# Kernel optimization log

Measured on AMD Instinct MI355X. Metric: run time of the kernel, lower is better.

## Reference

```python
import jax, jax.numpy as jnp
import numpy as np

SEQ_DIM = 256
PAIR_DIM = 128
N_HEADS = 8
HIDDEN = 32
B, L = 4, 512


def layer_norm(x, gamma, beta, eps=1e-5):
    mu = jnp.mean(x, axis=-1, keepdims=True)
    var = jnp.var(x, axis=-1, keepdims=True)
    return (x - mu) * jax.lax.rsqrt(var + eps) * gamma + beta


def setup_inputs() -> dict:
    key = jax.random.key(0)
    ks = jax.random.split(key, 12)
    d = N_HEADS * HIDDEN
    s = 0.02
    return {
        "seq": jax.random.normal(ks[0], (B, L, SEQ_DIM), jnp.float32),
        "pair": jax.random.normal(ks[1], (B, L, L, PAIR_DIM), jnp.float32),
        "ln_seq_g": jnp.ones((SEQ_DIM,), jnp.float32),
        "ln_seq_b": jnp.zeros((SEQ_DIM,), jnp.float32),
        "ln_pair_g": jnp.ones((PAIR_DIM,), jnp.float32),
        "ln_pair_b": jnp.zeros((PAIR_DIM,), jnp.float32),
        "W_b": jax.random.normal(ks[2], (PAIR_DIM, N_HEADS), jnp.float32) * s,
        "W_q": jax.random.normal(ks[3], (SEQ_DIM, d), jnp.float32) * s,
        "W_k": jax.random.normal(ks[4], (SEQ_DIM, d), jnp.float32) * s,
        "W_v": jax.random.normal(ks[5], (SEQ_DIM, d), jnp.float32) * s,
        "W_g": jax.random.normal(ks[6], (SEQ_DIM, d), jnp.float32) * s,
        "b_g": jnp.zeros((d,), jnp.float32),
        "W_o": jax.random.normal(ks[7], (d, SEQ_DIM), jnp.float32) * s,
        "b_o": jnp.zeros((SEQ_DIM,), jnp.float32),
    }


def reference(seq, pair, ln_seq_g, ln_seq_b, ln_pair_g, ln_pair_b,
              W_b, W_q, W_k, W_v, W_g, b_g, W_o, b_o):
    b, l, _ = seq.shape
    factor = 1.0 / np.sqrt(HIDDEN).astype(np.float32)
    s = layer_norm(seq, ln_seq_g, ln_seq_b)
    p = layer_norm(pair, ln_pair_g, ln_pair_b)
    Q = (s @ W_q).reshape(b, l, N_HEADS, HIDDEN)
    K = (s @ W_k).reshape(b, l, N_HEADS, HIDDEN)
    V = (s @ W_v).reshape(b, l, N_HEADS, HIDDEN)
    # pair bias: [b, i, j, n] -> [b, n, i, j]
    bias = jnp.einsum('bijp,pn->bnij', p, W_b)
    att = jnp.einsum('binh,bjnh->bnij', Q, K) * factor + bias
    att = jax.nn.softmax(att, axis=-1)
    gate = jax.nn.sigmoid(s @ W_g + b_g).reshape(b, l, N_HEADS, HIDDEN)
    out = jnp.einsum('bnij,bjnh->binh', att, V) * gate
    out = out.reshape(b, l, N_HEADS * HIDDEN)
    return out @ W_o + b_o
```

## Files before the change

kernel.cpp:

```cpp
#include <hip/hip_runtime.h>
#include <math.h>

#define NB 4
#define NL 512
#define SD 256
#define PD 128
#define NH 8
#define HD 32

#define OFF_Q    0
#define OFF_K    (524288)
#define OFF_V    (524288*2)
#define OFF_G    (524288*3)
#define OFF_PRE  (524288*4)
#define OFF_BIAS (524288*5)

#define SEL8(a, f, out) do { \
  float _s0 = ((f)&1) ? a[1] : a[0]; \
  float _s1 = ((f)&1) ? a[3] : a[2]; \
  float _s2 = ((f)&1) ? a[5] : a[4]; \
  float _s3 = ((f)&1) ? a[7] : a[6]; \
  float _t0 = ((f)&2) ? _s1 : _s0; \
  float _t1 = ((f)&2) ? _s3 : _s2; \
  out = ((f)&4) ? _t1 : _t0; \
} while(0)

__global__ __launch_bounds__(256) void k_mega(
    const float* __restrict__ seq, const float* __restrict__ lsg, const float* __restrict__ lsb,
    const float* __restrict__ lpg, const float* __restrict__ lpb, const float* __restrict__ Wb,
    const float* __restrict__ Wq, const float* __restrict__ Wk, const float* __restrict__ Wv,
    const float* __restrict__ Wg, const float* __restrict__ bg, const float* __restrict__ pair,
    float* __restrict__ Qw, float* __restrict__ Kw, float* __restrict__ Vw, float* __restrict__ Gw,
    float* __restrict__ biasw) {
  __shared__ __align__(16) float As[256*36];
  int t = threadIdx.x;
  int blk = blockIdx.x;

  if (blk < 512) {
    int m0 = (blk >> 3) * 32;
    int y = blk & 7;
    {
      int r = t >> 3, c0 = t & 7;
      const float* srow = seq + (size_t)(m0 + r) * 256;
      float4 v[8];
      float s = 0.f, sq = 0.f;
#pragma unroll
      for (int qq = 0; qq < 8; ++qq) {
        v[qq] = *(const float4*)(srow + 4*(c0 + 8*qq));
        s += v[qq].x + v[qq].y + v[qq].z + v[qq].w;
        sq = fmaf(v[qq].x, v[qq].x, sq); sq = fmaf(v[qq].y, v[qq].y, sq);
        sq = fmaf(v[qq].z, v[qq].z, sq); sq = fmaf(v[qq].w, v[qq].w, sq);
      }
#pragma unroll
      for (int mm = 1; mm < 8; mm <<= 1) { s += __shfl_xor(s, mm); sq += __shfl_xor(sq, mm); }
      float mu = s * (1.f/256.f);
      float var = sq * (1.f/256.f) - mu*mu;
      float rstd = rsqrtf(var + 1e-5f);
#pragma unroll
      for (int qq = 0; qq < 8; ++qq) {
        int c4 = c0 + 8*qq;
        float4 g  = *(const float4*)(lsg + 4*c4);
        float4 bb = *(const float4*)(lsb + 4*c4);
        float* dp = As + 4*c4*36 + r;
        dp[0]   = (v[qq].x - mu)*rstd*g.x + bb.x;
        dp[36]  = (v[qq].y - mu)*rstd*g.y + bb.y;
        dp[72]  = (v[qq].z - mu)*rstd*g.z + bb.z;
        dp[108] = (v[qq].w - mu)*rstd*g.w + bb.w;
      }
    }
    __syncthreads();
    const float* Wm = (y < 2) ? Wq : (y < 4) ? Wk : (y < 6) ? Wv : Wg;
    int cb = (y & 1) * 128;
    int rg = t >> 5, cg = t & 31;
    const float* bp = Wm + cb + 4*cg;
    const float* ap = As + 4*rg;
    float4 a0 = {0,0,0,0}, a1 = {0,0,0,0}, a2 = {0,0,0,0}, a3 = {0,0,0,0};
#pragma unroll 4
    for (int p = 0; p < 256; ++p) {
      float4 a  = *(const float4*)(ap + p*36);
      float4 bv = *(const float4*)(bp + p*256);
      a0.x = fmaf(a.x, bv.x, a0.x); a0.y = fmaf(a.x, bv.y, a0.y);
      a0.z = fmaf(a.x, bv.z, a0.z); a0.w = fmaf(a.x, bv.w, a0.w);
      a1.x = fmaf(a.y, bv.x, a1.x); a1.y = fmaf(a.y, bv.y, a1.y);
      a1.z = fmaf(a.y, bv.z, a1.z); a1.w = fmaf(a.y, bv.w, a1.w);
      a2.x = fmaf(a.z, bv.x, a2.x); a2.y = fmaf(a.z, bv.y, a2.y);
      a2.z = fmaf(a.z, bv.z, a2.z); a2.w = fmaf(a.z, bv.w, a2.w);
      a3.x = fmaf(a.w, bv.x, a3.x); a3.y = fmaf(a.w, bv.y, a3.y);
      a3.z = fmaf(a.w, bv.z, a3.z); a3.w = fmaf(a.w, bv.w, a3.w);
    }
    int mat = y >> 1;
    int col = cb + 4*cg;
    float* outp = (mat == 0) ? Qw : (mat == 1) ? Kw : (mat == 2) ? Vw : Gw;
    if (mat == 0) {
      const float qs = 0.17677669529663687f;
      a0.x*=qs; a0.y*=qs; a0.z*=qs; a0.w*=qs;
      a1.x*=qs; a1.y*=qs; a1.z*=qs; a1.w*=qs;
      a2.x*=qs; a2.y*=qs; a2.z*=qs; a2.w*=qs;
      a3.x*=qs; a3.y*=qs; a3.z*=qs; a3.w*=qs;
    }
    if (mat == 3) {
      float4 g4 = *(const float4*)(bg + col);
      a0.x = 1.f/(1.f+__expf(-(a0.x+g4.x))); a0.y = 1.f/(1.f+__expf(-(a0.y+g4.y)));
      a0.z = 1.f/(1.f+__expf(-(a0.z+g4.z))); a0.w = 1.f/(1.f+__expf(-(a0.w+g4.w)));
      a1.x = 1.f/(1.f+__expf(-(a1.x+g4.x))); a1.y = 1.f/(1.f+__expf(-(a1.y+g4.y)));
      a1.z = 1.f/(1.f+__expf(-(a1.z+g4.z))); a1.w = 1.f/(1.f+__expf(-(a1.w+g4.w)));
      a2.x = 1.f/(1.f+__expf(-(a2.x+g4.x))); a2.y = 1.f/(1.f+__expf(-(a2.y+g4.y)));
      a2.z = 1.f/(1.f+__expf(-(a2.z+g4.z))); a2.w = 1.f/(1.f+__expf(-(a2.w+g4.w)));
      a3.x = 1.f/(1.f+__expf(-(a3.x+g4.x))); a3.y = 1.f/(1.f+__expf(-(a3.y+g4.y)));
      a3.z = 1.f/(1.f+__expf(-(a3.z+g4.z))); a3.w = 1.f/(1.f+__expf(-(a3.w+g4.w)));
    }
    int orow = m0 + 4*rg;
    *(float4*)(outp + (size_t)(orow+0)*256 + col) = a0;
    *(float4*)(outp + (size_t)(orow+1)*256 + col) = a1;
    *(float4*)(outp + (size_t)(orow+2)*256 + col) = a2;
    *(float4*)(outp + (size_t)(orow+3)*256 + col) = a3;
    return;
  }

  int bb2 = blk - 512;
  int b = bb2 >> 9, i = bb2 & 511;
  int lane = t & 63, w = t >> 6;
  int grp = lane >> 4, f = lane & 15;

  float wb[64], wp[64];
  {
    const float* WbA = Wb + f*32;
    const float* WbB = Wb + (64 + 4*f)*8;
#pragma unroll
    for (int q = 0; q < 4; ++q) {
      float4 u0 = *(const float4*)(WbA + q*8);
      float4 u1 = *(const float4*)(WbA + q*8 + 4);
      wb[q*8+0]=u0.x; wb[q*8+1]=u0.y; wb[q*8+2]=u0.z; wb[q*8+3]=u0.w;
      wb[q*8+4]=u1.x; wb[q*8+5]=u1.y; wb[q*8+6]=u1.z; wb[q*8+7]=u1.w;
      float4 z0 = *(const float4*)(WbB + q*8);
      float4 z1 = *(const float4*)(WbB + q*8 + 4);
      wb[(4+q)*8+0]=z0.x; wb[(4+q)*8+1]=z0.y; wb[(4+q)*8+2]=z0.z; wb[(4+q)*8+3]=z0.w;
      wb[(4+q)*8+4]=z1.x; wb[(4+q)*8+5]=z1.y; wb[(4+q)*8+6]=z1.z; wb[(4+q)*8+7]=z1.w;
    }
  }
  float gl[8], bl[8];
  {
    float4 ga  = *(const float4*)(lpg + 4*f);
    float4 gb4 = *(const float4*)(lpg + 64 + 4*f);
    float4 ba  = *(const float4*)(lpb + 4*f);
    float4 bb4 = *(const float4*)(lpb + 64 + 4*f);
    gl[0]=ga.x; gl[1]=ga.y; gl[2]=ga.z; gl[3]=ga.w;
    gl[4]=gb4.x; gl[5]=gb4.y; gl[6]=gb4.z; gl[7]=gb4.w;
    bl[0]=ba.x; bl[1]=ba.y; bl[2]=ba.z; bl[3]=ba.w;
    bl[4]=bb4.x; bl[5]=bb4.y; bl[6]=bb4.z; bl[7]=bb4.w;
  }
  float cg[8] = {0,0,0,0,0,0,0,0}, cbv[8] = {0,0,0,0,0,0,0,0};
#pragma unroll
  for (int kk = 0; kk < 8; ++kk) {
#pragma unroll
    for (int n = 0; n < 8; ++n) {
      wp[kk*8+n] = gl[kk] * wb[kk*8+n];
      cg[n]  += wp[kk*8+n];
      cbv[n] = fmaf(bl[kk], wb[kk*8+n], cbv[n]);
    }
  }
#pragma unroll
  for (int mm = 1; mm < 16; mm <<= 1) {
#pragma unroll
    for (int n = 0; n < 8; ++n) {
      cg[n]  += __shfl_xor(cg[n],  mm);
      cbv[n] += __shfl_xor(cbv[n], mm);
    }
  }
  float cgsel, cbsel;
  SEL8(cg, f, cgsel);
  SEL8(cbv, f, cbsel);

  const float* prow0 = pair + (size_t)(b*512 + i) * (512*128);
  float* bw0 = biasw + (size_t)(b*8)*262144 + (size_t)i*512;
  for (int it = 0; it < 32; ++it) {
    int j = 16*it + 4*w + grp;
    const float* row = prow0 + (size_t)j*128;
    float4 x0 = *(const float4*)(row + 4*f);
    float4 x1 = *(const float4*)(row + 64 + 4*f);
    float xs[8] = {x0.x,x0.y,x0.z,x0.w, x1.x,x1.y,x1.z,x1.w};
    float s = 0.f, sq = 0.f;
    float dd[8] = {0,0,0,0,0,0,0,0};
#pragma unroll
    for (int kk = 0; kk < 8; ++kk) {
      s += xs[kk];
      sq = fmaf(xs[kk], xs[kk], sq);
#pragma unroll
      for (int n = 0; n < 8; ++n) dd[n] = fmaf(xs[kk], wp[kk*8+n], dd[n]);
    }
#pragma unroll
    for (int mm = 1; mm < 16; mm <<= 1) {
      s  += __shfl_xor(s,  mm);
      sq += __shfl_xor(sq, mm);
#pragma unroll
      for (int n = 0; n < 8; ++n) dd[n] += __shfl_xor(dd[n], mm);
    }
    float mu = s * (1.f/128.f);
    float var = fmaf(sq, 1.f/128.f, -mu*mu);
    float rstd = rsqrtf(var + 1e-5f);
    if (f < 8) {
      float dv;
      SEL8(dd, f, dv);
      bw0[(size_t)f*262144 + j] = fmaf(rstd, fmaf(-mu, cgsel, dv), cbsel);
    }
  }
}

__global__ __launch_bounds__(256) void k_attn(
    const float* __restrict__ Qw, const float* __restrict__ Kw, const float* __restrict__ Vw,
    const float* __restrict__ Gw, const float* __restrict__ biasw, float* __restrict__ prew) {
  __shared__ __align__(16) float sm[18496];
  float* Kl = sm;
  float* Vl = sm + 9248;
  int t = threadIdx.x;
  int b = blockIdx.x >> 6;
  int i0 = (blockIdx.x & 63) << 3;
  int lane = t & 63, w = t >> 6;
  int i = lane >> 3, n = lane & 7;
  int qrow = b*512 + i0 + i;
  float4 q[8];
  const float* qp = Qw + (size_t)qrow*256 + n*32;
#pragma unroll
  for (int x = 0; x < 8; ++x) q[x] = *(const float4*)(qp + 4*x);
  const float* brow = biasw + (size_t)((b*8 + n)*512 + i0 + i)*512 + 8*w;
  float4 acc[8];
#pragma unroll
  for (int x = 0; x < 8; ++x) acc[x] = make_float4(0.f,0.f,0.f,0.f);
  float m = -1e30f, l = 0.f;
  int sr = t >> 3, sc = t & 7;
  const float* kbase = Kw + (size_t)(b*512 + sr)*256 + 4*sc;
  const float* vbase = Vw + (size_t)(b*512 + sr)*256 + 4*sc;
  float* kd = Kl + 36*sr + 4*sc;
  float* vd = Vl + 36*sr + 4*sc;
  for (int tt = 0; tt < 16; ++tt) {
    int j0 = tt*32;
    const float* ks = kbase + (size_t)j0*256;
    const float* vs = vbase + (size_t)j0*256;
#pragma unroll
    for (int s = 0; s < 8; ++s)
      *(float4*)(kd + 1156*s) = *(const float4*)(ks + 32*s);
#pragma unroll
    for (int s = 0; s < 8; ++s)
      *(float4*)(vd + 1156*s) = *(const float4*)(vs + 32*s);
    __syncthreads();
    float4 b0 = *(const float4*)(brow + j0);
    float4 b1 = *(const float4*)(brow + j0 + 4);
    float bb[8] = {b0.x,b0.y,b0.z,b0.w,b1.x,b1.y,b1.z,b1.w};
    float lg[8];
    const float* kp0 = Kl + 1156*n + 36*(8*w);
#pragma unroll
    for (int jj = 0; jj < 8; ++jj) {
      const float* kp = kp0 + 36*jj;
      float d0 = 0.f;
#pragma unroll
      for (int x = 0; x < 8; ++x) {
        float4 kk = *(const float4*)(kp + 4*x);
        d0 = fmaf(q[x].x, kk.x, d0);
        d0 = fmaf(q[x].y, kk.y, d0);
        d0 = fmaf(q[x].z, kk.z, d0);
        d0 = fmaf(q[x].w, kk.w, d0);
      }
      lg[jj] = d0 + bb[jj];
    }
    float tm = lg[0];
#pragma unroll
    for (int jj = 1; jj < 8; ++jj) tm = fmaxf(tm, lg[jj]);
    if (tm > m) {
      float nm = tm;
      float scl = __expf(m - nm);
      l *= scl;
#pragma unroll
      for (int x = 0; x < 8; ++x) {
        acc[x].x *= scl; acc[x].y *= scl; acc[x].z *= scl; acc[x].w *= scl;
      }
      m = nm;
    }
    const float* vp0 = Vl + 1156*n + 36*(8*w);
#pragma unroll
    for (int jj = 0; jj < 8; ++jj) {
      float p = __expf(lg[jj] - m);
      l += p;
      const float* vp = vp0 + 36*jj;
#pragma unroll
      for (int x = 0; x < 8; ++x) {
        float4 vv = *(const float4*)(vp + 4*x);
        acc[x].x = fmaf(p, vv.x, acc[x].x);
        acc[x].y = fmaf(p, vv.y, acc[x].y);
        acc[x].z = fmaf(p, vv.z, acc[x].z);
        acc[x].w = fmaf(p, vv.w, acc[x].w);
      }
    }
    __syncthreads();
  }
  float* me = sm + t*37;
  me[0] = m; me[1] = l;
#pragma unroll
  for (int x = 0; x < 8; ++x) {
    me[2+4*x+0] = acc[x].x; me[2+4*x+1] = acc[x].y;
    me[2+4*x+2] = acc[x].z; me[2+4*x+3] = acc[x].w;
  }
  __syncthreads();
  if (w == 0) {
    float mw[4], lw[4];
    float M = -1e30f;
#pragma unroll
    for (int v4 = 0; v4 < 4; ++v4) {
      const float* pe = sm + (v4*64 + lane)*37;
      mw[v4] = pe[0]; lw[v4] = pe[1];
      M = fmaxf(M, mw[v4]);
    }
    float Lsum = 0.f, ew[4];
#pragma unroll
    for (int v4 = 0; v4 < 4; ++v4) { ew[v4] = __expf(mw[v4] - M); Lsum = fmaf(lw[v4], ew[v4], Lsum); }
    float inv = 1.f / Lsum;
    float o[32];
#pragma unroll
    for (int h = 0; h < 32; ++h) o[h] = 0.f;
#pragma unroll
    for (int v4 = 0; v4 < 4; ++v4) {
      const float* pe = sm + (v4*64 + lane)*37 + 2;
      float e = ew[v4];
#pragma unroll
      for (int h = 0; h < 32; ++h) o[h] = fmaf(pe[h], e, o[h]);
    }
    const float* gp = Gw + (size_t)qrow*256 + n*32;
    float* op = prew + (size_t)qrow*256 + n*32;
#pragma unroll
    for (int x = 0; x < 8; ++x) {
      float4 g4 = *(const float4*)(gp + 4*x);
      float4 r;
      r.x = o[4*x+0]*inv*g4.x;
      r.y = o[4*x+1]*inv*g4.y;
      r.z = o[4*x+2]*inv*g4.z;
      r.w = o[4*x+3]*inv*g4.w;
      *(float4*)(op + 4*x) = r;
    }
  }
}

__global__ __launch_bounds__(256) void k_out(
    const float* __restrict__ prew, const float* __restrict__ Wo, const float* __restrict__ bo,
    float* __restrict__ out) {
  __shared__ __align__(16) float As[256*36];
  int t = threadIdx.x;
  int m0 = blockIdx.x * 32;
  int y = blockIdx.y;
  {
    int r = t >> 3, c0 = t & 7;
    const float* srow = prew + (size_t)(m0 + r)*256;
#pragma unroll
    for (int qq = 0; qq < 8; ++qq) {
      int c4 = c0 + 8*qq;
      float4 v = *(const float4*)(srow + 4*c4);
      float* dp = As + 4*c4*36 + r;
      dp[0] = v.x; dp[36] = v.y; dp[72] = v.z; dp[108] = v.w;
    }
  }
  __syncthreads();
  int cb = y*128;
  int rg = t >> 5, cg = t & 31;
  int col = cb + 4*cg;
  const float* bp = Wo + col;
  const float* ap = As + 4*rg;
  float4 a0 = {0,0,0,0}, a1 = {0,0,0,0}, a2 = {0,0,0,0}, a3 = {0,0,0,0};
#pragma unroll 4
  for (int p = 0; p < 256; ++p) {
    float4 a  = *(const float4*)(ap + p*36);
    float4 bv = *(const float4*)(bp + p*256);
    a0.x = fmaf(a.x, bv.x, a0.x); a0.y = fmaf(a.x, bv.y, a0.y);
    a0.z = fmaf(a.x, bv.z, a0.z); a0.w = fmaf(a.x, bv.w, a0.w);
    a1.x = fmaf(a.y, bv.x, a1.x); a1.y = fmaf(a.y, bv.y, a1.y);
    a1.z = fmaf(a.y, bv.z, a1.z); a1.w = fmaf(a.y, bv.w, a1.w);
    a2.x = fmaf(a.z, bv.x, a2.x); a2.y = fmaf(a.z, bv.y, a2.y);
    a2.z = fmaf(a.z, bv.z, a2.z); a2.w = fmaf(a.z, bv.w, a2.w);
    a3.x = fmaf(a.w, bv.x, a3.x); a3.y = fmaf(a.w, bv.y, a3.y);
    a3.z = fmaf(a.w, bv.z, a3.z); a3.w = fmaf(a.w, bv.w, a3.w);
  }
  float4 b4 = *(const float4*)(bo + col);
  a0.x += b4.x; a0.y += b4.y; a0.z += b4.z; a0.w += b4.w;
  a1.x += b4.x; a1.y += b4.y; a1.z += b4.z; a1.w += b4.w;
  a2.x += b4.x; a2.y += b4.y; a2.z += b4.z; a2.w += b4.w;
  a3.x += b4.x; a3.y += b4.y; a3.z += b4.z; a3.w += b4.w;
  int orow = m0 + 4*rg;
  *(float4*)(out + (size_t)(orow+0)*256 + col) = a0;
  *(float4*)(out + (size_t)(orow+1)*256 + col) = a1;
  *(float4*)(out + (size_t)(orow+2)*256 + col) = a2;
  *(float4*)(out + (size_t)(orow+3)*256 + col) = a3;
}

extern "C" void kernel_launch(void* const* d_in, const int* in_sizes, int n_in,
                              void* d_out, int out_size, void* d_ws, size_t ws_size,
                              hipStream_t stream) {
  const float* seq  = (const float*)d_in[0];
  const float* pair = (const float*)d_in[1];
  const float* lsg  = (const float*)d_in[2];
  const float* lsb  = (const float*)d_in[3];
  const float* lpg  = (const float*)d_in[4];
  const float* lpb  = (const float*)d_in[5];
  const float* Wb   = (const float*)d_in[6];
  const float* Wq   = (const float*)d_in[7];
  const float* Wk   = (const float*)d_in[8];
  const float* Wv   = (const float*)d_in[9];
  const float* Wg   = (const float*)d_in[10];
  const float* bg   = (const float*)d_in[11];
  const float* Wo   = (const float*)d_in[12];
  const float* bo   = (const float*)d_in[13];
  float* ws   = (float*)d_ws;
  float* Qw   = ws + OFF_Q;
  float* Kw   = ws + OFF_K;
  float* Vw   = ws + OFF_V;
  float* Gw   = ws + OFF_G;
  float* prew = ws + OFF_PRE;
  float* biasw= ws + OFF_BIAS;
  float* out  = (float*)d_out;

  hipLaunchKernelGGL(k_mega, dim3(2560), dim3(256), 0, stream,
                     seq, lsg, lsb, lpg, lpb, Wb, Wq, Wk, Wv, Wg, bg, pair,
                     Qw, Kw, Vw, Gw, biasw);
  hipLaunchKernelGGL(k_attn, dim3(256), dim3(256), 0, stream,
                     Qw, Kw, Vw, Gw, biasw, prew);
  hipLaunchKernelGGL(k_out, dim3(64, 2), dim3(256), 0, stream,
                     prew, Wo, bo, out);
}
```

Baseline: 251.1 us.

## Rewrite attention kernel with double-buffered tiles and DPP reductions in bias pass

The attention kernel is replaced by a 512-thread version. It double-buffers the K, V and bias tiles through registers into shared memory, processes two query rows per thread, and merges the per-lane softmax partials with DPP lane moves instead of a shared-memory scratch reduction. The pair-bias pass swaps its shuffle-xor reductions for DPP row reductions and software-prefetches the next pair row. Its weight setup is simplified, and it gets launch_bounds(256,3). The aim is to overlap global loads with compute and cut cross-lane reduction cost, at the price of higher register and shared-memory pressure.

```diff
diff --git a/kernel.cpp b/kernel.cpp
--- a/kernel.cpp
+++ b/kernel.cpp
@@ -1,12 +1,5 @@
 #include <hip/hip_runtime.h>
 #include <math.h>
-
-#define NB 4
-#define NL 512
-#define SD 256
-#define PD 128
-#define NH 8
-#define HD 32
 
 #define OFF_Q    0
 #define OFF_K    (524288)
@@ -14,6 +7,20 @@
 #define OFF_G    (524288*3)
 #define OFF_PRE  (524288*4)
 #define OFF_BIAS (524288*5)
+
+template <int CTRL>
+__device__ __forceinline__ float dpp_mov(float x) {
+  return __int_as_float(__builtin_amdgcn_update_dpp(0, __float_as_int(x), CTRL, 0xF, 0xF, true));
+}
+template <int CTRL>
+__device__ __forceinline__ float dpp_add(float x) { return x + dpp_mov<CTRL>(x); }
+__device__ __forceinline__ float red16(float v) {
+  v = dpp_add<0xB1>(v);
+  v = dpp_add<0x4E>(v);
+  v = dpp_add<0x141>(v);
+  v = dpp_add<0x140>(v);
+  return v;
+}
 
 #define SEL8(a, f, out) do { \
   float _s0 = ((f)&1) ? a[1] : a[0]; \
@@ -25,7 +32,39 @@
   out = ((f)&4) ? _t1 : _t0; \
 } while(0)
 
-__global__ __launch_bounds__(256) void k_mega(
+__device__ __forceinline__ float4 sel8_f4(const float4* a, int f) {
+  float4 s0 = (f&1) ? a[1] : a[0];
+  float4 s1 = (f&1) ? a[3] : a[2];
+  float4 s2 = (f&1) ? a[5] : a[4];
+  float4 s3 = (f&1) ? a[7] : a[6];
+  float4 t0 = (f&2) ? s1 : s0;
+  float4 t1 = (f&2) ? s3 : s2;
+  return (f&4) ? t1 : t0;
+}
+
+__device__ __forceinline__ float dot4(float4 a, float4 b, float acc) {
+  acc = fmaf(a.x, b.x, acc); acc = fmaf(a.y, b.y, acc);
+  acc = fmaf(a.z, b.z, acc); return fmaf(a.w, b.w, acc);
+}
+
+template <int CTRL>
+__device__ __forceinline__ void merge_dpp(float& m, float& l, float4* acc) {
+  float m2 = dpp_mov<CTRL>(m);
+  float l2 = dpp_mov<CTRL>(l);
+  float M = fmaxf(m, m2);
+  float ea = __expf(m - M), eb = __expf(m2 - M);
+  l = l*ea + l2*eb;
+#pragma unroll
+  for (int x = 0; x < 8; ++x) {
+    acc[x].x = acc[x].x*ea + dpp_mov<CTRL>(acc[x].x)*eb;
+    acc[x].y = acc[x].y*ea + dpp_mov<CTRL>(acc[x].y)*eb;
+    acc[x].z = acc[x].z*ea + dpp_mov<CTRL>(acc[x].z)*eb;
+    acc[x].w = acc[x].w*ea + dpp_mov<CTRL>(acc[x].w)*eb;
+  }
+  m = M;
+}
+
+__global__ __launch_bounds__(256, 3) void k_mega(
     const float* __restrict__ seq, const float* __restrict__ lsg, const float* __restrict__ lsb,
     const float* __restrict__ lpg, const float* __restrict__ lpb, const float* __restrict__ Wb,
     const float* __restrict__ Wq, const float* __restrict__ Wk, const float* __restrict__ Wv,
@@ -71,8 +110,8 @@
     __syncthreads();
     const float* Wm = (y < 2) ? Wq : (y < 4) ? Wk : (y < 6) ? Wv : Wg;
     int cb = (y & 1) * 128;
-    int rg = t >> 5, cg = t & 31;
-    const float* bp = Wm + cb + 4*cg;
+    int rg = t >> 5, cg2 = t & 31;
+    const float* bp = Wm + cb + 4*cg2;
     const float* ap = As + 4*rg;
     float4 a0 = {0,0,0,0}, a1 = {0,0,0,0}, a2 = {0,0,0,0}, a3 = {0,0,0,0};
 #pragma unroll 4
@@ -89,7 +128,7 @@
       a3.z = fmaf(a.w, bv.z, a3.z); a3.w = fmaf(a.w, bv.w, a3.w);
     }
     int mat = y >> 1;
-    int col = cb + 4*cg;
+    int col = cb + 4*cg2;
     float* outp = (mat == 0) ? Qw : (mat == 1) ? Kw : (mat == 2) ? Vw : Gw;
     if (mat == 0) {
       const float qs = 0.17677669529663687f;
@@ -122,79 +161,78 @@
   int lane = t & 63, w = t >> 6;
   int grp = lane >> 4, f = lane & 15;
 
-  float wb[64], wp[64];
-  {
-    const float* WbA = Wb + f*32;
-    const float* WbB = Wb + (64 + 4*f)*8;
-#pragma unroll
-    for (int q = 0; q < 4; ++q) {
-      float4 u0 = *(const float4*)(WbA + q*8);
-      float4 u1 = *(const float4*)(WbA + q*8 + 4);
-      wb[q*8+0]=u0.x; wb[q*8+1]=u0.y; wb[q*8+2]=u0.z; wb[q*8+3]=u0.w;
-      wb[q*8+4]=u1.x; wb[q*8+5]=u1.y; wb[q*8+6]=u1.z; wb[q*8+7]=u1.w;
-      float4 z0 = *(const float4*)(WbB + q*8);
-      float4 z1 = *(const float4*)(WbB + q*8 + 4);
-      wb[(4+q)*8+0]=z0.x; wb[(4+q)*8+1]=z0.y; wb[(4+q)*8+2]=z0.z; wb[(4+q)*8+3]=z0.w;
-      wb[(4+q)*8+4]=z1.x; wb[(4+q)*8+5]=z1.y; wb[(4+q)*8+6]=z1.z; wb[(4+q)*8+7]=z1.w;
-    }
-  }
-  float gl[8], bl[8];
-  {
-    float4 ga  = *(const float4*)(lpg + 4*f);
-    float4 gb4 = *(const float4*)(lpg + 64 + 4*f);
-    float4 ba  = *(const float4*)(lpb + 4*f);
-    float4 bb4 = *(const float4*)(lpb + 64 + 4*f);
-    gl[0]=ga.x; gl[1]=ga.y; gl[2]=ga.z; gl[3]=ga.w;
-    gl[4]=gb4.x; gl[5]=gb4.y; gl[6]=gb4.z; gl[7]=gb4.w;
-    bl[0]=ba.x; bl[1]=ba.y; bl[2]=ba.z; bl[3]=ba.w;
-    bl[4]=bb4.x; bl[5]=bb4.y; bl[6]=bb4.z; bl[7]=bb4.w;
-  }
+  float wp[64];
   float cg[8] = {0,0,0,0,0,0,0,0}, cbv[8] = {0,0,0,0,0,0,0,0};
 #pragma unroll
-  for (int kk = 0; kk < 8; ++kk) {
-#pragma unroll
-    for (int n = 0; n < 8; ++n) {
-      wp[kk*8+n] = gl[kk] * wb[kk*8+n];
-      cg[n]  += wp[kk*8+n];
-      cbv[n] = fmaf(bl[kk], wb[kk*8+n], cbv[n]);
-    }
-  }
-#pragma unroll
-  for (int mm = 1; mm < 16; mm <<= 1) {
-#pragma unroll
-    for (int n = 0; n < 8; ++n) {
-      cg[n]  += __shfl_xor(cg[n],  mm);
-      cbv[n] += __shfl_xor(cbv[n], mm);
-    }
-  }
+  for (int q = 0; q < 4; ++q) {
+    int kA = 4*f + q, kB = 64 + 4*f + q;
+    float gA = lpg[kA], bA = lpb[kA];
+    float gB = lpg[kB], bB = lpb[kB];
+    float4 uA0 = *(const float4*)(Wb + kA*8);
+    float4 uA1 = *(const float4*)(Wb + kA*8 + 4);
+    float4 uB0 = *(const float4*)(Wb + kB*8);
+    float4 uB1 = *(const float4*)(Wb + kB*8 + 4);
+    wp[q*8+0] = gA*uA0.x; cg[0] += wp[q*8+0]; cbv[0] = fmaf(bA, uA0.x, cbv[0]);
+    wp[q*8+1] = gA*uA0.y; cg[1] += wp[q*8+1]; cbv[1] = fmaf(bA, uA0.y, cbv[1]);
+    wp[q*8+2] = gA*uA0.z; cg[2] += wp[q*8+2]; cbv[2] = fmaf(bA, uA0.z, cbv[2]);
+    wp[q*8+3] = gA*uA0.w; cg[3] += wp[q*8+3]; cbv[3] = fmaf(bA, uA0.w, cbv[3]);
+    wp[q*8+4] = gA*uA1.x; cg[4] += wp[q*8+4]; cbv[4] = fmaf(bA, uA1.x, cbv[4]);
+    wp[q*8+5] = gA*uA1.y; cg[5] += wp[q*8+5]; cbv[5] = fmaf(bA, uA1.y, cbv[5]);
+    wp[q*8+6] = gA*uA1.z; cg[6] += wp[q*8+6]; cbv[6] = fmaf(bA, uA1.z, cbv[6]);
+    wp[q*8+7] = gA*uA1.w; cg[7] += wp[q*8+7]; cbv[7] = fmaf(bA, uA1.w, cbv[7]);
+    int qb8 = (4+q)*8;
+    wp[qb8+0] = gB*uB0.x; cg[0] += wp[qb8+0]; cbv[0] = fmaf(bB, uB0.x, cbv[0]);
+    wp[qb8+1] = gB*uB0.y; cg[1] += wp[qb8+1]; cbv[1] = fmaf(bB, uB0.y, cbv[1]);
+    wp[qb8+2] = gB*uB0.z; cg[2] += wp[qb8+2]; cbv[2] = fmaf(bB, uB0.z, cbv[2]);
+    wp[qb8+3] = gB*uB0.w; cg[3] += wp[qb8+3]; cbv[3] = fmaf(bB, uB0.w, cbv[3]);
+    wp[qb8+4] = gB*uB1.x; cg[4] += wp[qb8+4]; cbv[4] = fmaf(bB, uB1.x, cbv[4]);
+    wp[qb8+5] = gB*uB1.y; cg[5] += wp[qb8+5]; cbv[5] = fmaf(bB, uB1.y, cbv[5]);
+    wp[qb8+6] = gB*uB1.z; cg[6] += wp[qb8+6]; cbv[6] = fmaf(bB, uB1.z, cbv[6]);
+    wp[qb8+7] = gB*uB1.w; cg[7] += wp[qb8+7]; cbv[7] = fmaf(bB, uB1.w, cbv[7]);
+  }
+#pragma unroll
+  for (int n2 = 0; n2 < 8; ++n2) { cg[n2] = red16(cg[n2]); cbv[n2] = red16(cbv[n2]); }
   float cgsel, cbsel;
   SEL8(cg, f, cgsel);
   SEL8(cbv, f, cbsel);
 
   const float* prow0 = pair + (size_t)(b*512 + i) * (512*128);
   float* bw0 = biasw + (size_t)(b*8)*262144 + (size_t)i*512;
+
+  int j = 4*w + grp;
+  const float* rp = prow0 + (size_t)j*128 + 4*f;
+  float4 x0 = *(const float4*)rp;
+  float4 x1 = *(const float4*)(rp + 64);
+#pragma unroll 2
   for (int it = 0; it < 32; ++it) {
-    int j = 16*it + 4*w + grp;
-    const float* row = prow0 + (size_t)j*128;
-    float4 x0 = *(const float4*)(row + 4*f);
-    float4 x1 = *(const float4*)(row + 64 + 4*f);
-    float xs[8] = {x0.x,x0.y,x0.z,x0.w, x1.x,x1.y,x1.z,x1.w};
-    float s = 0.f, sq = 0.f;
-    float dd[8] = {0,0,0,0,0,0,0,0};
-#pragma unroll
-    for (int kk = 0; kk < 8; ++kk) {
-      s += xs[kk];
-      sq = fmaf(xs[kk], xs[kk], sq);
-#pragma unroll
-      for (int n = 0; n < 8; ++n) dd[n] = fmaf(xs[kk], wp[kk*8+n], dd[n]);
-    }
-#pragma unroll
-    for (int mm = 1; mm < 16; mm <<= 1) {
-      s  += __shfl_xor(s,  mm);
-      sq += __shfl_xor(sq, mm);
-#pragma unroll
-      for (int n = 0; n < 8; ++n) dd[n] += __shfl_xor(dd[n], mm);
-    }
+    float4 y0, y1;
+    if (it < 31) {
+      const float* rn = rp + 16*128;
+      y0 = *(const float4*)rn;
+      y1 = *(const float4*)(rn + 64);
+    }
+    float s  = x0.x + x0.y + x0.z + x0.w + x1.x + x1.y + x1.z + x1.w;
+    float sq = x0.x*x0.x;
+    sq = fmaf(x0.y, x0.y, sq); sq = fmaf(x0.z, x0.z, sq); sq = fmaf(x0.w, x0.w, sq);
+    sq = fmaf(x1.x, x1.x, sq); sq = fmaf(x1.y, x1.y, sq);
+    sq = fmaf(x1.z, x1.z, sq); sq = fmaf(x1.w, x1.w, sq);
+    float dd[8];
+#pragma unroll
+    for (int n2 = 0; n2 < 8; ++n2) {
+      float d = x0.x * wp[n2];
+      d = fmaf(x0.y, wp[8+n2],  d);
+      d = fmaf(x0.z, wp[16+n2], d);
+      d = fmaf(x0.w, wp[24+n2], d);
+      d = fmaf(x1.x, wp[32+n2], d);
+      d = fmaf(x1.y, wp[40+n2], d);
+      d = fmaf(x1.z, wp[48+n2], d);
+      d = fmaf(x1.w, wp[56+n2], d);
+      dd[n2] = d;
+    }
+    s  = red16(s);
+    sq = red16(sq);
+#pragma unroll
+    for (int n2 = 0; n2 < 8; ++n2) dd[n2] = red16(dd[n2]);
     float mu = s * (1.f/128.f);
     float var = fmaf(sq, 1.f/128.f, -mu*mu);
     float rstd = rsqrtf(var + 1e-5f);
@@ -203,137 +241,200 @@
       SEL8(dd, f, dv);
       bw0[(size_t)f*262144 + j] = fmaf(rstd, fmaf(-mu, cgsel, dv), cbsel);
     }
-  }
-}
-
-__global__ __launch_bounds__(256) void k_attn(
+    j += 16; rp += 16*128;
+    x0 = y0; x1 = y1;
+  }
+}
+
+#define KVS 260
+#define BBS 36
+
+__global__ __launch_bounds__(512, 2) void k_attn2(
     const float* __restrict__ Qw, const float* __restrict__ Kw, const float* __restrict__ Vw,
     const float* __restrict__ Gw, const float* __restrict__ biasw, float* __restrict__ prew) {
-  __shared__ __align__(16) float sm[18496];
-  float* Kl = sm;
-  float* Vl = sm + 9248;
-  int t = threadIdx.x;
-  int b = blockIdx.x >> 6;
-  int i0 = (blockIdx.x & 63) << 3;
-  int lane = t & 63, w = t >> 6;
-  int i = lane >> 3, n = lane & 7;
-  int qrow = b*512 + i0 + i;
-  float4 q[8];
-  const float* qp = Qw + (size_t)qrow*256 + n*32;
-#pragma unroll
-  for (int x = 0; x < 8; ++x) q[x] = *(const float4*)(qp + 4*x);
-  const float* brow = biasw + (size_t)((b*8 + n)*512 + i0 + i)*512 + 8*w;
-  float4 acc[8];
-#pragma unroll
-  for (int x = 0; x < 8; ++x) acc[x] = make_float4(0.f,0.f,0.f,0.f);
-  float m = -1e30f, l = 0.f;
-  int sr = t >> 3, sc = t & 7;
-  const float* kbase = Kw + (size_t)(b*512 + sr)*256 + 4*sc;
-  const float* vbase = Vw + (size_t)(b*512 + sr)*256 + 4*sc;
-  float* kd = Kl + 36*sr + 4*sc;
-  float* vd = Vl + 36*sr + 4*sc;
+  __shared__ __align__(16) float Kb[2][32*KVS];
+  __shared__ __align__(16) float Vb[2][32*KVS];
+  __shared__ __align__(16) float Bb[2][64*BBS];
+  __shared__ __align__(16) float scr[4*8*68];
+
+  int t = threadIdx.x, lane = t & 63, w = t >> 6;
+  int b = blockIdx.x >> 6, i0 = (blockIdx.x & 63) << 3;
+  int n = lane >> 3, js = lane & 7;
+  int ip = w & 3, jset = w >> 2;
+  int ila = 2*ip, ilb = ila + 1;
+  size_t qra = (size_t)(b*512 + i0 + ila);
+  size_t qrb = qra + 1;
+
+  float4 qa[8], qb[8];
+  {
+    const float* pa = Qw + qra*256 + n*32;
+    const float* pb = Qw + qrb*256 + n*32;
+#pragma unroll
+    for (int x = 0; x < 8; ++x) { qa[x] = *(const float4*)(pa + 4*x); qb[x] = *(const float4*)(pb + 4*x); }
+  }
+  float4 acca[8], accb[8];
+#pragma unroll
+  for (int x = 0; x < 8; ++x) { acca[x] = make_float4(0,0,0,0); accb[x] = make_float4(0,0,0,0); }
+  float ma = -1e30f, la = 0.f, mb2 = -1e30f, lb2 = 0.f;
+
+  const float* Kg = Kw + (size_t)(b*512)*256;
+  const float* Vg = Vw + (size_t)(b*512)*256;
+  int sidx = 8*w + (lane >> 3);
+  int s_il = sidx >> 3, s_n = sidx & 7;
+  const float* bgsrc = biasw + (size_t)((b*8 + s_n)*512 + i0 + s_il)*512 + 4*(lane & 7);
+
+  float4 sk[4], sv[4], sb;
+
+#define STAGE_LOAD(tn) { \
+    const float* ks_ = Kg + (size_t)((tn)*32 + 4*w)*256 + 4*lane; \
+    const float* vs_ = Vg + (size_t)((tn)*32 + 4*w)*256 + 4*lane; \
+    sk[0] = *(const float4*)(ks_);        sk[1] = *(const float4*)(ks_ + 256); \
+    sk[2] = *(const float4*)(ks_ + 512);  sk[3] = *(const float4*)(ks_ + 768); \
+    sv[0] = *(const float4*)(vs_);        sv[1] = *(const float4*)(vs_ + 256); \
+    sv[2] = *(const float4*)(vs_ + 512);  sv[3] = *(const float4*)(vs_ + 768); \
+    sb = *(const float4*)(bgsrc + (tn)*32); \
+  }
+#define STAGE_WRITE(tn) { int bf_ = (tn) & 1; \
+    float* kd_ = &Kb[bf_][(4*w)*KVS + 4*lane]; \
+    *(float4*)(kd_)         = sk[0]; *(float4*)(kd_ + KVS)   = sk[1]; \
+    *(float4*)(kd_ + 2*KVS) = sk[2]; *(float4*)(kd_ + 3*KVS) = sk[3]; \
+    float* vd_ = &Vb[bf_][(4*w)*KVS + 4*lane]; \
+    *(float4*)(vd_)         = sv[0]; *(float4*)(vd_ + KVS)   = sv[1]; \
+    *(float4*)(vd_ + 2*KVS) = sv[2]; *(float4*)(vd_ + 3*KVS) = sv[3]; \
+    *(float4*)(&Bb[bf_][sidx*BBS + 4*(lane & 7)]) = sb; \
+  }
+
+  STAGE_LOAD(0);
+  STAGE_WRITE(0);
+  __syncthreads();
+
+  int jl0 = jset*16 + js;
   for (int tt = 0; tt < 16; ++tt) {
-    int j0 = tt*32;
-    const float* ks = kbase + (size_t)j0*256;
-    const float* vs = vbase + (size_t)j0*256;
-#pragma unroll
-    for (int s = 0; s < 8; ++s)
-      *(float4*)(kd + 1156*s) = *(const float4*)(ks + 32*s);
-#pragma unroll
-    for (int s = 0; s < 8; ++s)
-      *(float4*)(vd + 1156*s) = *(const float4*)(vs + 32*s);
-    __syncthreads();
-    float4 b0 = *(const float4*)(brow + j0);
-    float4 b1 = *(const float4*)(brow + j0 + 4);
-    float bb[8] = {b0.x,b0.y,b0.z,b0.w,b1.x,b1.y,b1.z,b1.w};
-    float lg[8];
-    const float* kp0 = Kl + 1156*n + 36*(8*w);
-#pragma unroll
-    for (int jj = 0; jj < 8; ++jj) {
-      const float* kp = kp0 + 36*jj;
-      float d0 = 0.f;
+    int cur = tt & 1;
+    if (tt < 15) STAGE_LOAD(tt+1);
+
+    const float* Kt = Kb[cur];
+    const float* Vt = Vb[cur];
+    const float* Bt = Bb[cur];
+
+    float lga0, lga1, lgb0, lgb1;
+    {
+      const float* kp = Kt + jl0*KVS + n*32;
+      float da = 0.f, db = 0.f;
 #pragma unroll
       for (int x = 0; x < 8; ++x) {
         float4 kk = *(const float4*)(kp + 4*x);
-        d0 = fmaf(q[x].x, kk.x, d0);
-        d0 = fmaf(q[x].y, kk.y, d0);
-        d0 = fmaf(q[x].z, kk.z, d0);
-        d0 = fmaf(q[x].w, kk.w, d0);
-      }
-      lg[jj] = d0 + bb[jj];
-    }
-    float tm = lg[0];
-#pragma unroll
-    for (int jj = 1; jj < 8; ++jj) tm = fmaxf(tm, lg[jj]);
-    if (tm > m) {
-      float nm = tm;
-      float scl = __expf(m - nm);
-      l *= scl;
+        da = dot4(qa[x], kk, da); db = dot4(qb[x], kk, db);
+      }
+      lga0 = da + Bt[(ila*8 + n)*BBS + jl0];
+      lgb0 = db + Bt[(ilb*8 + n)*BBS + jl0];
+    }
+    {
+      const float* kp = Kt + (jl0+8)*KVS + n*32;
+      float da = 0.f, db = 0.f;
 #pragma unroll
       for (int x = 0; x < 8; ++x) {
-        acc[x].x *= scl; acc[x].y *= scl; acc[x].z *= scl; acc[x].w *= scl;
-      }
-      m = nm;
-    }
-    const float* vp0 = Vl + 1156*n + 36*(8*w);
-#pragma unroll
-    for (int jj = 0; jj < 8; ++jj) {
-      float p = __expf(lg[jj] - m);
-      l += p;
-      const float* vp = vp0 + 36*jj;
+        float4 kk = *(const float4*)(kp + 4*x);
+        da = dot4(qa[x], kk, da); db = dot4(qb[x], kk, db);
+      }
+      lga1 = da + Bt[(ila*8 + n)*BBS + jl0 + 8];
+      lgb1 = db + Bt[(ilb*8 + n)*BBS + jl0 + 8];
+    }
+    {
+      float tm = fmaxf(lga0, lga1);
+      float M = fmaxf(ma, tm);
+      float sc = __expf(ma - M);
+      la *= sc;
+#pragma unroll
+      for (int x = 0; x < 8; ++x) {
+        acca[x].x *= sc; acca[x].y *= sc; acca[x].z *= sc; acca[x].w *= sc;
+      }
+      ma = M;
+    }
+    {
+      float tm = fmaxf(lgb0, lgb1);
+      float M = fmaxf(mb2, tm);
+      float sc = __expf(mb2 - M);
+      lb2 *= sc;
+#pragma unroll
+      for (int x = 0; x < 8; ++x) {
+        accb[x].x *= sc; accb[x].y *= sc; accb[x].z *= sc; accb[x].w *= sc;
+      }
+      mb2 = M;
+    }
+    float pa0 = __expf(lga0 - ma), pa1 = __expf(lga1 - ma);
+    float pb0 = __expf(lgb0 - mb2), pb1 = __expf(lgb1 - mb2);
+    la += pa0 + pa1; lb2 += pb0 + pb1;
+    {
+      const float* vp = Vt + jl0*KVS + n*32;
 #pragma unroll
       for (int x = 0; x < 8; ++x) {
         float4 vv = *(const float4*)(vp + 4*x);
-        acc[x].x = fmaf(p, vv.x, acc[x].x);
-        acc[x].y = fmaf(p, vv.y, acc[x].y);
-        acc[x].z = fmaf(p, vv.z, acc[x].z);
-        acc[x].w = fmaf(p, vv.w, acc[x].w);
-      }
-    }
+        acca[x].x = fmaf(pa0, vv.x, acca[x].x); acca[x].y = fmaf(pa0, vv.y, acca[x].y);
+        acca[x].z = fmaf(pa0, vv.z, acca[x].z); acca[x].w = fmaf(pa0, vv.w, acca[x].w);
+        accb[x].x = fmaf(pb0, vv.x, accb[x].x); accb[x].y = fmaf(pb0, vv.y, accb[x].y);
+        accb[x].z = fmaf(pb0, vv.z, accb[x].z); accb[x].w = fmaf(pb0, vv.w, accb[x].w);
+      }
+    }
+    {
+      const float* vp = Vt + (jl0+8)*KVS + n*32;
+#pragma unroll
+      for (int x = 0; x < 8; ++x) {
+        float4 vv = *(const float4*)(vp + 4*x);
+        acca[x].x = fmaf(pa1, vv.x, acca[x].x); acca[x].y = fmaf(pa1, vv.y, acca[x].y);
+        acca[x].z = fmaf(pa1, vv.z, acca[x].z); acca[x].w = fmaf(pa1, vv.w, acca[x].w);
+        accb[x].x = fmaf(pb1, vv.x, accb[x].x); accb[x].y = fmaf(pb1, vv.y, accb[x].y);
+        accb[x].z = fmaf(pb1, vv.z, accb[x].z); accb[x].w = fmaf(pb1, vv.w, accb[x].w);
+      }
+    }
+
+    if (tt < 15) STAGE_WRITE(tt+1);
     __syncthreads();
   }
-  float* me = sm + t*37;
-  me[0] = m; me[1] = l;
-#pragma unroll
-  for (int x = 0; x < 8; ++x) {
-    me[2+4*x+0] = acc[x].x; me[2+4*x+1] = acc[x].y;
-    me[2+4*x+2] = acc[x].z; me[2+4*x+3] = acc[x].w;
+
+  merge_dpp<0xB1>(ma, la, acca);   merge_dpp<0xB1>(mb2, lb2, accb);
+  merge_dpp<0x4E>(ma, la, acca);   merge_dpp<0x4E>(mb2, lb2, accb);
+  merge_dpp<0x141>(ma, la, acca);  merge_dpp<0x141>(mb2, lb2, accb);
+
+  float4 fa = sel8_f4(acca, js);
+  float4 fb = sel8_f4(accb, js);
+
+  if (jset == 1) {
+    int base = (ip*8 + n)*68;
+    *(float4*)(scr + base + 4*js) = fa;
+    *(float4*)(scr + base + 32 + 4*js) = fb;
+    if (js == 0) { scr[base+64] = ma; scr[base+65] = la; scr[base+66] = mb2; scr[base+67] = lb2; }
   }
   __syncthreads();
-  if (w == 0) {
-    float mw[4], lw[4];
-    float M = -1e30f;
-#pragma unroll
-    for (int v4 = 0; v4 < 4; ++v4) {
-      const float* pe = sm + (v4*64 + lane)*37;
-      mw[v4] = pe[0]; lw[v4] = pe[1];
-      M = fmaxf(M, mw[v4]);
-    }
-    float Lsum = 0.f, ew[4];
-#pragma unroll
-    for (int v4 = 0; v4 < 4; ++v4) { ew[v4] = __expf(mw[v4] - M); Lsum = fmaf(lw[v4], ew[v4], Lsum); }
-    float inv = 1.f / Lsum;
-    float o[32];
-#pragma unroll
-    for (int h = 0; h < 32; ++h) o[h] = 0.f;
-#pragma unroll
-    for (int v4 = 0; v4 < 4; ++v4) {
-      const float* pe = sm + (v4*64 + lane)*37 + 2;
-      float e = ew[v4];
-#pragma unroll
-      for (int h = 0; h < 32; ++h) o[h] = fmaf(pe[h], e, o[h]);
-    }
-    const float* gp = Gw + (size_t)qrow*256 + n*32;
-    float* op = prew + (size_t)qrow*256 + n*32;
-#pragma unroll
-    for (int x = 0; x < 8; ++x) {
-      float4 g4 = *(const float4*)(gp + 4*x);
+  if (jset == 0) {
+    int base = (ip*8 + n)*68;
+    float4 a2 = *(const float4*)(scr + base + 4*js);
+    float4 b2 = *(const float4*)(scr + base + 32 + 4*js);
+    float m2a = scr[base+64], l2a = scr[base+65];
+    float m2b = scr[base+66], l2b = scr[base+67];
+    {
+      float M = fmaxf(ma, m2a);
+      float ea = __expf(ma - M), eb = __expf(m2a - M);
+      float inv = 1.f / (la*ea + l2a*eb);
+      float4 g4 = *(const float4*)(Gw + qra*256 + n*32 + 4*js);
       float4 r;
-      r.x = o[4*x+0]*inv*g4.x;
-      r.y = o[4*x+1]*inv*g4.y;
-      r.z = o[4*x+2]*inv*g4.z;
-      r.w = o[4*x+3]*inv*g4.w;
-      *(float4*)(op + 4*x) = r;
+      r.x = (fa.x*ea + a2.x*eb) * inv * g4.x;
+      r.y = (fa.y*ea + a2.y*eb) * inv * g4.y;
+      r.z = (fa.z*ea + a2.z*eb) * inv * g4.z;
+      r.w = (fa.w*ea + a2.w*eb) * inv * g4.w;
+      *(float4*)(prew + qra*256 + n*32 + 4*js) = r;
+    }
+    {
+      float M = fmaxf(mb2, m2b);
+      float ea = __expf(mb2 - M), eb = __expf(m2b - M);
+      float inv = 1.f / (lb2*ea + l2b*eb);
+      float4 g4 = *(const float4*)(Gw + qrb*256 + n*32 + 4*js);
+      float4 r;
+      r.x = (fb.x*ea + b2.x*eb) * inv * g4.x;
+      r.y = (fb.y*ea + b2.y*eb) * inv * g4.y;
+      r.z = (fb.z*ea + b2.z*eb) * inv * g4.z;
+      r.w = (fb.w*ea + b2.w*eb) * inv * g4.w;
+      *(float4*)(prew + qrb*256 + n*32 + 4*js) = r;
     }
   }
 }
@@ -358,8 +459,8 @@
   }
   __syncthreads();
   int cb = y*128;
-  int rg = t >> 5, cg = t & 31;
-  int col = cb + 4*cg;
+  int rg = t >> 5, cg2 = t & 31;
+  int col = cb + 4*cg2;
   const float* bp = Wo + col;
   const float* ap = As + 4*rg;
   float4 a0 = {0,0,0,0}, a1 = {0,0,0,0}, a2 = {0,0,0,0}, a3 = {0,0,0,0};
@@ -417,7 +518,7 @@
   hipLaunchKernelGGL(k_mega, dim3(2560), dim3(256), 0, stream,
                      seq, lsg, lsb, lpg, lpb, Wb, Wq, Wk, Wv, Wg, bg, pair,
                      Qw, Kw, Vw, Gw, biasw);
-  hipLaunchKernelGGL(k_attn, dim3(256), dim3(256), 0, stream,
+  hipLaunchKernelGGL(k_attn2, dim3(256), dim3(512), 0, stream,
                      Qw, Kw, Vw, Gw, biasw, prew);
   hipLaunchKernelGGL(k_out, dim3(64, 2), dim3(256), 0, stream,
                      prew, Wo, bo, out);
```

Measured after the change: 242.5 us. 3.4% less time.
